# Performance work log

Hardware: AMD Instinct MI355X
Metric: run time of the kernel (lower is better)

## Reference

```python
import jax, jax.numpy as jnp
import numpy as np

DIM = 1024
DEPTH = 4
HEADS = 16
DIM_HEAD = 64
MLP = 4096
INNER = HEADS * DIM_HEAD  # == DIM, so to_out projection present
SCALE = DIM_HEAD ** -0.5
EPS = 1e-5


def layernorm(x, g, b):
    mu = jnp.mean(x, axis=-1, keepdims=True)
    var = jnp.var(x, axis=-1, keepdims=True)
    return (x - mu) * jax.lax.rsqrt(var + EPS) * g + b


def setup_inputs() -> dict:
    key = jax.random.key(0)
    ks = jax.random.split(key, 12)
    B, N = 4, 1024
    s = lambda fan: 1.0 / np.sqrt(fan)
    inp = {
        "x": jax.random.normal(ks[0], (B, N, DIM), jnp.float32),
        "Wqkv": jax.random.normal(ks[1], (DEPTH, DIM, 3 * INNER), jnp.float32) * s(DIM),
        "Wout": jax.random.normal(ks[2], (DEPTH, INNER, DIM), jnp.float32) * s(INNER),
        "bout": jnp.zeros((DEPTH, DIM), jnp.float32),
        "ln1_g": jnp.ones((DEPTH, DIM), jnp.float32),
        "ln1_b": jnp.zeros((DEPTH, DIM), jnp.float32),
        "W1": jax.random.normal(ks[3], (DEPTH, DIM, MLP), jnp.float32) * s(DIM),
        "b1": jnp.zeros((DEPTH, MLP), jnp.float32),
        "W2": jax.random.normal(ks[4], (DEPTH, MLP, DIM), jnp.float32) * s(MLP),
        "b2": jnp.zeros((DEPTH, DIM), jnp.float32),
        "ln2_g": jnp.ones((DEPTH, DIM), jnp.float32),
        "ln2_b": jnp.zeros((DEPTH, DIM), jnp.float32),
        "masks_np": jax.random.randint(ks[5], (B, N), 0, 2, jnp.int32),
        "masks_bert": jax.random.randint(ks[6], (B, N), 0, 2, jnp.int32),
    }
    return inp


def reference(x, Wqkv, Wout, bout, ln1_g, ln1_b, W1, b1, W2, b2, ln2_g, ln2_b,
              masks_np, masks_bert):
    B, N, _ = x.shape
    # pairwise mask: masks_np_[b,i,j] = masks_np[b,i] * masks_np[b,j]
    np_pair = (masks_np[:, :, None] * masks_np[:, None, :])[:, None, :, :]  # [B,1,N,N]
    bert_col = masks_bert[:, None, None, :]                                  # [B,1,1,N]
    for l in range(DEPTH):
        # --- PreNorm masked attention ---
        h = layernorm(x, ln1_g[l], ln1_b[l])
        qkv = h @ Wqkv[l]                                   # [B,N,3*INNER]
        q, k, v = jnp.split(qkv, 3, axis=-1)
        rs = lambda t: t.reshape(B, N, HEADS, DIM_HEAD).transpose(0, 2, 1, 3)
        q, k, v = rs(q), rs(k), rs(v)                       # [B,H,N,D]
        dots = jnp.einsum('bhid,bhjd->bhij', q, k) * SCALE  # [B,H,N,N]
        dots = jnp.where(np_pair == 0, -1000.0, dots)
        dots = jnp.where(bert_col == 1, -1000.0, dots)
        attn = jax.nn.softmax(dots, axis=-1)
        out = jnp.einsum('bhij,bhjd->bhid', attn, v)        # [B,H,N,D]
        out = out.transpose(0, 2, 1, 3).reshape(B, N, INNER)
        x = x + (out @ Wout[l] + bout[l])
        # --- PreNorm FFN ---
        h2 = layernorm(x, ln2_g[l], ln2_b[l])
        h2 = jax.nn.gelu(h2 @ W1[l] + b1[l], approximate=False)
        x = x + (h2 @ W2[l] + b2[l])
    return x
```

## Files before the change

### kernel.cpp

```cpp
#include <hip/hip_runtime.h>
#include <hip/hip_bf16.h>

#define DEPTH 4
#define HEADS 16
#define DIMH  64
#define DIM   1024
#define MLPD  4096
#define NTOK  1024
#define BATCH 4
#define ROWS  (BATCH*NTOK)
#define SCALE 0.125f

typedef float f32x4 __attribute__((ext_vector_type(4)));
typedef short s16x8 __attribute__((ext_vector_type(8)));

#define MFMA(a,b,c) __builtin_amdgcn_mfma_f32_16x16x32_bf16((a),(b),(c),0,0,0)

__device__ __forceinline__ unsigned short f2bf(float f){
  union{ __hip_bfloat16 h; unsigned short u; } x; x.h = __float2bfloat16(f); return x.u;
}
__device__ __forceinline__ float bf2f(unsigned short u){
  return __uint_as_float(((unsigned)u)<<16);
}

__device__ __forceinline__ void async16(const void* g, void* l){
  __builtin_amdgcn_global_load_lds(
      (const __attribute__((address_space(1))) void*)g,
      (__attribute__((address_space(3))) void*)l, 16, 0, 0);
}

__global__ __launch_bounds__(256) void wt_kernel(const float* __restrict__ src,
    unsigned short* __restrict__ dst, int K, int N)
{
  __shared__ float t[64][65];
  int n0 = blockIdx.x*64, k0 = blockIdx.y*64;
  src += (size_t)blockIdx.z*K*N;
  dst += (size_t)blockIdx.z*N*K;
  int tid = threadIdx.x;
  int r = tid>>4, c4 = (tid&15)*4;
#pragma unroll
  for (int p=0;p<4;p++){
    int row = r + p*16;
    float4 v = *(const float4*)(src + (size_t)(k0+row)*N + n0 + c4);
    t[c4+0][row]=v.x; t[c4+1][row]=v.y; t[c4+2][row]=v.z; t[c4+3][row]=v.w;
  }
  __syncthreads();
  int rn = tid>>2, ch = tid&3;
  unsigned short o[16];
#pragma unroll
  for (int i=0;i<16;i++) o[i] = f2bf(t[rn][ch*16+i]);
  uint4* d = (uint4*)(dst + (size_t)(n0+rn)*K + k0 + ch*16);
  d[0] = ((uint4*)o)[0]; d[1] = ((uint4*)o)[1];
}

__global__ __launch_bounds__(256) void ln_kernel(const float* __restrict__ x,
    const float* __restrict__ g, const float* __restrict__ b,
    unsigned short* __restrict__ h)
{
  int row  = blockIdx.x*4 + (threadIdx.x>>6);
  int lane = threadIdx.x & 63;
  const float* xr = x + (size_t)row*DIM;
  float4 v[4]; float s=0.f, ss=0.f;
#pragma unroll
  for (int c=0;c<4;c++){
    v[c] = *(const float4*)(xr + c*256 + lane*4);
    s  += v[c].x+v[c].y+v[c].z+v[c].w;
    ss += v[c].x*v[c].x+v[c].y*v[c].y+v[c].z*v[c].z+v[c].w*v[c].w;
  }
#pragma unroll
  for (int o=1;o<64;o<<=1){ s += __shfl_xor(s,o); ss += __shfl_xor(ss,o); }
  float mu  = s*(1.f/1024.f);
  float var = ss*(1.f/1024.f) - mu*mu;
  float rstd = rsqrtf(var + 1e-5f);
#pragma unroll
  for (int c=0;c<4;c++){
    float4 gg = *(const float4*)(g + c*256 + lane*4);
    float4 bb = *(const float4*)(b + c*256 + lane*4);
    ushort4 o;
    o.x = f2bf((v[c].x-mu)*rstd*gg.x + bb.x);
    o.y = f2bf((v[c].y-mu)*rstd*gg.y + bb.y);
    o.z = f2bf((v[c].z-mu)*rstd*gg.z + bb.z);
    o.w = f2bf((v[c].w-mu)*rstd*gg.w + bb.w);
    *(ushort4*)(h + (size_t)row*DIM + c*256 + lane*4) = o;
  }
}

__global__ __launch_bounds__(256) void vtrans_kernel(
    const unsigned short* __restrict__ qkv, unsigned short* __restrict__ vT)
{
  __shared__ float t[64][65];
  int n0 = blockIdx.x*64;
  int bh = blockIdx.y; int b = bh>>4, hh = bh&15;
  int tid = threadIdx.x;
  int r = tid>>4, c4 = (tid&15)*4;
#pragma unroll
  for (int p=0;p<4;p++){
    int row = r + p*16;
    ushort4 u = *(const ushort4*)(qkv + (size_t)(b*NTOK + n0 + row)*3072 + 2048 + hh*64 + c4);
    t[c4+0][row]=bf2f(u.x); t[c4+1][row]=bf2f(u.y); t[c4+2][row]=bf2f(u.z); t[c4+3][row]=bf2f(u.w);
  }
  __syncthreads();
  int rn = tid>>2, ch = tid&3;
  unsigned short o[16];
#pragma unroll
  for (int i=0;i<16;i++) o[i] = f2bf(t[rn][ch*16+i]);
  uint4* d = (uint4*)(vT + (size_t)(bh*64 + rn)*NTOK + n0 + ch*16);
  d[0] = ((uint4*)o)[0]; d[1] = ((uint4*)o)[1];
}

template<int BN, int EPI>
__global__ __launch_bounds__(256) void gemm_kernel(
    const unsigned short* __restrict__ A,
    const unsigned short* __restrict__ Bt,
    unsigned short* __restrict__ outb,
    float* __restrict__ outf,
    const float* __restrict__ res,
    const float* __restrict__ bias,
    int M, int N, int K, int ldout)
{
  constexpr int BM=128, BK=64;
  constexpr int NT = BN/32;
  __shared__ unsigned short As[BM*BK];
  __shared__ unsigned short Bs[BN*BK];
  int tid = threadIdx.x, lane = tid&63, w = tid>>6;
  int wm = w&1, wn = w>>1;

  int gn  = N/BN;
  int nwg = (M/BM)*gn;
  int bid = blockIdx.x;
  int id  = (nwg%8==0) ? ((bid&7)*(nwg>>3) + (bid>>3)) : bid;
  int m0 = (id/gn)*BM, n0 = (id%gn)*BN;

  f32x4 acc[4][NT] = {};

  for (int k0=0; k0<K; k0+=BK){
    __syncthreads();
#pragma unroll
    for (int i=0;i<4;i++){
      int off = w*4096 + i*1024 + lane*16;
      int row = off>>7, p = (off&127)>>4;
      async16(A + (size_t)(m0+row)*K + k0 + ((p^(row&7))<<3),
              (char*)As + w*4096 + i*1024);
    }
#pragma unroll
    for (int i=0;i<NT;i++){
      int off = w*(BN*32) + i*1024 + lane*16;
      int row = off>>7, p = (off&127)>>4;
      async16(Bt + (size_t)(n0+row)*K + k0 + ((p^(row&7))<<3),
              (char*)Bs + w*(BN*32) + i*1024);
    }
    __syncthreads();
#pragma unroll
    for (int ks=0;ks<2;ks++){
      s16x8 a[4], bfr[NT];
#pragma unroll
      for (int mt=0;mt<4;mt++){
        int row = wm*64 + mt*16 + (lane&15);
        int c = (ks*4 + (lane>>4)) ^ (row&7);
        a[mt] = *(const s16x8*)((const char*)As + row*128 + c*16);
      }
#pragma unroll
      for (int nt=0;nt<NT;nt++){
        int row = wn*(BN/2) + nt*16 + (lane&15);
        int c = (ks*4 + (lane>>4)) ^ (row&7);
        bfr[nt] = *(const s16x8*)((const char*)Bs + row*128 + c*16);
      }
#pragma unroll
      for (int mt=0;mt<4;mt++)
#pragma unroll
        for (int nt=0;nt<NT;nt++)
          acc[mt][nt] = MFMA(a[mt], bfr[nt], acc[mt][nt]);
    }
  }

#pragma unroll
  for (int mt=0;mt<4;mt++)
#pragma unroll
    for (int nt=0;nt<NT;nt++)
#pragma unroll
      for (int r=0;r<4;r++){
        int row = m0 + wm*64 + mt*16 + ((lane>>4)<<2) + r;
        int col = n0 + wn*(BN/2) + nt*16 + (lane&15);
        float v = acc[mt][nt][r];
        if (EPI==0){
          outb[(size_t)row*ldout + col] = f2bf(v);
        } else if (EPI==1){
          float t = v + res[(size_t)row*ldout + col] + bias[col];
          outf[(size_t)row*ldout + col] = t;
        } else {
          float t = v + bias[col];
          t = 0.5f*t*(1.f + erff(t*0.70710678118f));
          outb[(size_t)row*ldout + col] = f2bf(t);
        }
      }
}

__global__ __launch_bounds__(256) void attn_kernel(
    const unsigned short* __restrict__ qkv,
    const unsigned short* __restrict__ vT,
    const int* __restrict__ mnp, const int* __restrict__ mbert,
    unsigned short* __restrict__ outb)
{
  __shared__ unsigned short Ks[64*64];
  __shared__ unsigned short Vs[64*64];
  __shared__ unsigned short Pb[4][16*64];
  __shared__ float fm[NTOK];
  int qt = blockIdx.x, bh = blockIdx.y;
  int b = bh>>4, hh = bh&15;
  int tid = threadIdx.x, lane = tid&63, w = tid>>6;

  for (int j = tid; j < NTOK; j += 256)
    fm[j] = (mnp[b*NTOK+j]==0 || mbert[b*NTOK+j]==1) ? 1.f : 0.f;

  int iA = qt*64 + w*16 + (lane&15);
  s16x8 aq[2];
#pragma unroll
  for (int ks=0;ks<2;ks++)
    aq[ks] = *(const s16x8*)(qkv + (size_t)(b*NTOK+iA)*3072 + hh*64 + ks*32 + ((lane>>4)<<3));

  bool rowm[4]; float mreg[4], lsum[4]; f32x4 o[4];
#pragma unroll
  for (int r=0;r<4;r++){
    int i = qt*64 + w*16 + ((lane>>4)<<2) + r;
    rowm[r] = (mnp[b*NTOK+i]==0);
    mreg[r] = -1e30f; lsum[r] = 0.f;
    o[r] = f32x4{0.f,0.f,0.f,0.f};
  }

  for (int kc=0; kc<16; kc++){
    int j0 = kc*64;
    __syncthreads();
#pragma unroll
    for (int i=0;i<2;i++){
      int off = w*2048 + i*1024 + lane*16;
      int row = off>>7, p = (off&127)>>4;
      async16(qkv + (size_t)(b*NTOK + j0 + row)*3072 + 1024 + hh*64 + ((p^(row&7))<<3),
              (char*)Ks + w*2048 + i*1024);
      async16(vT + (size_t)(bh*64 + row)*NTOK + j0 + ((p^(row&7))<<3),
              (char*)Vs + w*2048 + i*1024);
    }
    __syncthreads();

    f32x4 sc[4];
#pragma unroll
    for (int jt=0;jt<4;jt++){
      sc[jt] = f32x4{0.f,0.f,0.f,0.f};
#pragma unroll
      for (int ks=0;ks<2;ks++){
        int row = jt*16 + (lane&15);
        int c = (ks*4 + (lane>>4)) ^ (row&7);
        s16x8 bk = *(const s16x8*)((const char*)Ks + row*128 + c*16);
        sc[jt] = MFMA(aq[ks], bk, sc[jt]);
      }
    }
#pragma unroll
    for (int jt=0;jt<4;jt++){
      float f = fm[j0 + jt*16 + (lane&15)];
#pragma unroll
      for (int r=0;r<4;r++){
        float s = sc[jt][r]*SCALE;
        sc[jt][r] = (f!=0.f || rowm[r]) ? -1000.f : s;
      }
    }
#pragma unroll
    for (int r=0;r<4;r++){
      float mx = fmaxf(fmaxf(sc[0][r],sc[1][r]), fmaxf(sc[2][r],sc[3][r]));
#pragma unroll
      for (int ofs=8;ofs>=1;ofs>>=1) mx = fmaxf(mx, __shfl_xor(mx, ofs));
      float mnew  = fmaxf(mreg[r], mx);
      float alpha = __expf(mreg[r]-mnew);
      mreg[r] = mnew;
      float rs = 0.f;
#pragma unroll
      for (int jt=0;jt<4;jt++){ float p = __expf(sc[jt][r]-mnew); sc[jt][r]=p; rs+=p; }
#pragma unroll
      for (int ofs=8;ofs>=1;ofs>>=1) rs += __shfl_xor(rs, ofs);
      lsum[r] = lsum[r]*alpha + rs;
#pragma unroll
      for (int nt=0;nt<4;nt++) o[nt][r] *= alpha;
    }
#pragma unroll
    for (int jt=0;jt<4;jt++)
#pragma unroll
      for (int r=0;r<4;r++){
        int ir = ((lane>>4)<<2)+r, jc = jt*16+(lane&15);
        int byteoff = ir*128 + ((((jc>>3))^(ir&7))<<4) + ((jc&7)<<1);
        *((unsigned short*)((char*)Pb[w] + byteoff)) = f2bf(sc[jt][r]);
      }
#pragma unroll
    for (int ks=0;ks<2;ks++){
      int rowp = lane&15;
      int cp = (ks*4 + (lane>>4)) ^ (rowp&7);
      s16x8 ap = *(const s16x8*)((const char*)Pb[w] + rowp*128 + cp*16);
#pragma unroll
      for (int nt=0;nt<4;nt++){
        int d = nt*16 + (lane&15);
        int c = (ks*4 + (lane>>4)) ^ (d&7);
        s16x8 bv = *(const s16x8*)((const char*)Vs + d*128 + c*16);
        o[nt] = MFMA(ap, bv, o[nt]);
      }
    }
  }

#pragma unroll
  for (int r=0;r<4;r++){
    float inv = 1.f/lsum[r];
    int i = qt*64 + w*16 + ((lane>>4)<<2) + r;
#pragma unroll
    for (int nt=0;nt<4;nt++){
      int d = nt*16 + (lane&15);
      outb[(size_t)(b*NTOK+i)*DIM + hh*64 + d] = f2bf(o[nt][r]*inv);
    }
  }
}

extern "C" void kernel_launch(void* const* d_in, const int* in_sizes, int n_in,
                              void* d_out, int out_size, void* d_ws, size_t ws_size,
                              hipStream_t stream)
{
  const float* xin0 = (const float*)d_in[0];
  const float* Wqkv = (const float*)d_in[1];
  const float* Wout = (const float*)d_in[2];
  const float* bout = (const float*)d_in[3];
  const float* ln1g = (const float*)d_in[4];
  const float* ln1b = (const float*)d_in[5];
  const float* W1   = (const float*)d_in[6];
  const float* b1   = (const float*)d_in[7];
  const float* W2   = (const float*)d_in[8];
  const float* b2   = (const float*)d_in[9];
  const float* ln2g = (const float*)d_in[10];
  const float* ln2b = (const float*)d_in[11];
  const int*   mnp  = (const int*)d_in[12];
  const int*   mbt  = (const int*)d_in[13];
  float* out = (float*)d_out;

  unsigned short* Wqkv_t = (unsigned short*)d_ws;
  unsigned short* Wout_t = Wqkv_t + (size_t)4*3072*1024;
  unsigned short* W1_t   = Wout_t + (size_t)4*1024*1024;
  unsigned short* W2_t   = W1_t   + (size_t)4*4096*1024;
  float*          x      = (float*)(W2_t + (size_t)4*1024*4096);
  unsigned short* hbuf   = (unsigned short*)(x + (size_t)ROWS*DIM);
  unsigned short* qkvb   = hbuf  + (size_t)ROWS*DIM;
  unsigned short* vTb    = qkvb  + (size_t)ROWS*3072;
  unsigned short* attnb  = vTb   + (size_t)ROWS*DIM;
  unsigned short* gbuf   = attnb + (size_t)ROWS*DIM;

  wt_kernel<<<dim3(3072/64,1024/64,4),256,0,stream>>>(Wqkv, Wqkv_t, 1024, 3072);
  wt_kernel<<<dim3(1024/64,1024/64,4),256,0,stream>>>(Wout, Wout_t, 1024, 1024);
  wt_kernel<<<dim3(4096/64,1024/64,4),256,0,stream>>>(W1,   W1_t,   1024, 4096);
  wt_kernel<<<dim3(1024/64,4096/64,4),256,0,stream>>>(W2,   W2_t,   4096, 1024);

  for (int l=0;l<4;l++){
    const float* xres = (l==0) ? xin0 : x;
    ln_kernel<<<1024,256,0,stream>>>(xres, ln1g+l*DIM, ln1b+l*DIM, hbuf);
    gemm_kernel<128,0><<<768,256,0,stream>>>(hbuf, Wqkv_t + (size_t)l*3072*1024,
        qkvb, nullptr, nullptr, nullptr, ROWS, 3072, 1024, 3072);
    vtrans_kernel<<<dim3(16,64),256,0,stream>>>(qkvb, vTb);
    attn_kernel<<<dim3(16,64),256,0,stream>>>(qkvb, vTb, mnp, mbt, attnb);
    gemm_kernel<64,1><<<512,256,0,stream>>>(attnb, Wout_t + (size_t)l*1024*1024,
        nullptr, x, xres, bout+l*DIM, ROWS, 1024, 1024, 1024);
    ln_kernel<<<1024,256,0,stream>>>(x, ln2g+l*DIM, ln2b+l*DIM, hbuf);
    gemm_kernel<128,2><<<1024,256,0,stream>>>(hbuf, W1_t + (size_t)l*4096*1024,
        gbuf, nullptr, nullptr, b1+l*MLPD, ROWS, 4096, 1024, 4096);
    float* xo = (l==3) ? out : x;
    gemm_kernel<64,1><<<512,256,0,stream>>>(gbuf, W2_t + (size_t)l*1024*4096,
        nullptr, xo, x, b2+l*DIM, ROWS, 1024, 4096, 1024);
  }
}
```

Before: 1.258 ms.

## Add 256x256 pipelined GEMM for QKV/FFN1 and double-buffer attention K/V loads

```diff
diff --git a/kernel.cpp b/kernel.cpp
--- a/kernel.cpp
+++ b/kernel.cpp
@@ -195,14 +195,149 @@
       }
 }
 
+template<int EPI>
+__global__ __launch_bounds__(512,2) void gemm256_kernel(
+    const unsigned short* __restrict__ A,
+    const unsigned short* __restrict__ Bt,
+    unsigned short* __restrict__ outb,
+    const float* __restrict__ bias,
+    int M, int N, int K, int ldout)
+{
+  __shared__ unsigned short lds[2][2][256*64];
+  const int tid = threadIdx.x, lane = tid&63, w = tid>>6;
+  const int wm = w>>2, wn = w&3;
+  const int gn = N>>8;
+  const int nwg = (M>>8)*gn;
+  const int q = nwg>>3, r = nwg&7;
+  const int xc = blockIdx.x&7, od = blockIdx.x>>3;
+  const int id = (xc<r ? xc*(q+1) : r*(q+1)+(xc-r)*q) + od;
+  const int m0 = (id/gn)<<8, n0 = (id%gn)<<8;
+  const int nkt = K>>6;
+
+  f32x4 acc[8][4] = {};
+  s16x8 af[8][2];
+  s16x8 bf[2][2];
+
+  auto stage = [&](int bsel, int half, int kt){
+    const unsigned short* src = (half<2) ? A : Bt;
+    const int base0 = (half<2) ? m0 : n0;
+    const int rbase = (half&1)<<7;
+    char* dstbase = (char*)lds[bsel][half>>1] + (rbase<<7);
+#pragma unroll
+    for (int i=0;i<2;i++){
+      int off  = ((w<<1)+i)<<10;
+      int loff = off + lane*16;
+      int row  = loff>>7, p = (loff&127)>>4;
+      async16(src + (size_t)(base0+rbase+row)*K + (kt<<6) + ((p^(row&7))<<3),
+              dstbase + off);
+    }
+  };
+
+#define LDA(mt,ks) { int rw=(wm<<7)+((mt)<<4)+(lane&15); int pc=(((ks)<<2)+(lane>>4))^(rw&7); \
+  af[mt][ks] = *(const s16x8*)((const char*)lds[cur][0] + rw*128 + (pc<<4)); }
+#define LDB(j,nt,ks) { int rw=(wn<<6)+((nt)<<4)+(lane&15); int pc=(((ks)<<2)+(lane>>4))^(rw&7); \
+  bf[j][ks] = *(const s16x8*)((const char*)lds[cur][1] + rw*128 + (pc<<4)); }
+
+  stage(0,0,0); stage(0,1,0); stage(0,2,0); stage(0,3,0);
+  stage(1,0,1); stage(1,1,1);
+  asm volatile("s_waitcnt vmcnt(4)" ::: "memory");
+  __builtin_amdgcn_s_barrier();
+
+  for (int t=0; t<nkt; ++t){
+    const int cur = t&1, nxt = cur^1;
+#pragma unroll
+    for (int mt=0;mt<4;mt++){ LDA(mt,0); LDA(mt,1); }
+#pragma unroll
+    for (int nt=0;nt<2;nt++){ LDB(nt,nt,0); LDB(nt,nt,1); }
+    if (t+1<nkt) stage(nxt,2,t+1);
+    __builtin_amdgcn_s_barrier();
+    asm volatile("s_waitcnt lgkmcnt(0)" ::: "memory");
+    __builtin_amdgcn_sched_barrier(0);
+    __builtin_amdgcn_s_setprio(1);
+#pragma unroll
+    for (int mt=0;mt<4;mt++)
+#pragma unroll
+      for (int nt=0;nt<2;nt++){
+        acc[mt][nt] = MFMA(af[mt][0], bf[nt][0], acc[mt][nt]);
+        acc[mt][nt] = MFMA(af[mt][1], bf[nt][1], acc[mt][nt]);
+      }
+    __builtin_amdgcn_s_setprio(0);
+    __builtin_amdgcn_s_barrier();
+#pragma unroll
+    for (int mt=4;mt<8;mt++){ LDA(mt,0); LDA(mt,1); }
+    if (t+1<nkt) stage(nxt,3,t+1);
+    __builtin_amdgcn_s_barrier();
+    asm volatile("s_waitcnt lgkmcnt(0)" ::: "memory");
+    __builtin_amdgcn_sched_barrier(0);
+    __builtin_amdgcn_s_setprio(1);
+#pragma unroll
+    for (int mt=4;mt<8;mt++)
+#pragma unroll
+      for (int nt=0;nt<2;nt++){
+        acc[mt][nt] = MFMA(af[mt][0], bf[nt][0], acc[mt][nt]);
+        acc[mt][nt] = MFMA(af[mt][1], bf[nt][1], acc[mt][nt]);
+      }
+    __builtin_amdgcn_s_setprio(0);
+    __builtin_amdgcn_s_barrier();
+#pragma unroll
+    for (int nt=0;nt<2;nt++){ LDB(nt,nt+2,0); LDB(nt,nt+2,1); }
+    if (t+2<nkt) stage(cur,0,t+2);
+    __builtin_amdgcn_s_barrier();
+    asm volatile("s_waitcnt lgkmcnt(0)" ::: "memory");
+    __builtin_amdgcn_sched_barrier(0);
+    __builtin_amdgcn_s_setprio(1);
+#pragma unroll
+    for (int mt=0;mt<4;mt++)
+#pragma unroll
+      for (int nt=0;nt<2;nt++){
+        acc[mt][nt+2] = MFMA(af[mt][0], bf[nt][0], acc[mt][nt+2]);
+        acc[mt][nt+2] = MFMA(af[mt][1], bf[nt][1], acc[mt][nt+2]);
+      }
+    __builtin_amdgcn_s_setprio(0);
+    __builtin_amdgcn_s_barrier();
+    if (t+2<nkt) stage(cur,1,t+2);
+    __builtin_amdgcn_s_barrier();
+    __builtin_amdgcn_s_setprio(1);
+#pragma unroll
+    for (int mt=4;mt<8;mt++)
+#pragma unroll
+      for (int nt=0;nt<2;nt++){
+        acc[mt][nt+2] = MFMA(af[mt][0], bf[nt][0], acc[mt][nt+2]);
+        acc[mt][nt+2] = MFMA(af[mt][1], bf[nt][1], acc[mt][nt+2]);
+      }
+    __builtin_amdgcn_s_setprio(0);
+    if (t+2<nkt) asm volatile("s_waitcnt vmcnt(4)" ::: "memory");
+    else         asm volatile("s_waitcnt vmcnt(0)" ::: "memory");
+    __builtin_amdgcn_s_barrier();
+  }
+#undef LDA
+#undef LDB
+
+#pragma unroll
+  for (int mt=0;mt<8;mt++)
+#pragma unroll
+    for (int nt=0;nt<4;nt++)
+#pragma unroll
+      for (int rr=0;rr<4;rr++){
+        int row = m0 + (wm<<7) + (mt<<4) + ((lane>>4)<<2) + rr;
+        int col = n0 + (wn<<6) + (nt<<4) + (lane&15);
+        float v = acc[mt][nt][rr];
+        if (EPI==2){
+          v += bias[col];
+          v = 0.5f*v*(1.f + erff(v*0.70710678118f));
+        }
+        outb[(size_t)row*ldout + col] = f2bf(v);
+      }
+}
+
 __global__ __launch_bounds__(256) void attn_kernel(
     const unsigned short* __restrict__ qkv,
     const unsigned short* __restrict__ vT,
     const int* __restrict__ mnp, const int* __restrict__ mbert,
     unsigned short* __restrict__ outb)
 {
-  __shared__ unsigned short Ks[64*64];
-  __shared__ unsigned short Vs[64*64];
+  __shared__ unsigned short Ks[2][64*64];
+  __shared__ unsigned short Vs[2][64*64];
   __shared__ unsigned short Pb[4][16*64];
   __shared__ float fm[NTOK];
   int qt = blockIdx.x, bh = blockIdx.y;
@@ -226,22 +361,34 @@
     mreg[r] = -1e30f; lsum[r] = 0.f;
     o[r] = f32x4{0.f,0.f,0.f,0.f};
   }
+  __syncthreads();
+
+  auto stageKV = [&](int bufi, int kc){
+    int j0 = kc<<6;
+#pragma unroll
+    for (int i=0;i<2;i++){
+      int off  = w*2048 + i*1024;
+      int loff = off + lane*16;
+      int row  = loff>>7, p = (loff&127)>>4;
+      async16(qkv + (size_t)(b*NTOK + j0 + row)*3072 + 1024 + hh*64 + ((p^(row&7))<<3),
+              (char*)Ks[bufi] + off);
+      async16(vT + (size_t)(bh*64 + row)*NTOK + j0 + ((p^(row&7))<<3),
+              (char*)Vs[bufi] + off);
+    }
+  };
+
+  stageKV(0,0);
 
   for (int kc=0; kc<16; kc++){
+    int cur = kc&1;
     int j0 = kc*64;
-    __syncthreads();
-#pragma unroll
-    for (int i=0;i<2;i++){
-      int off = w*2048 + i*1024 + lane*16;
-      int row = off>>7, p = (off&127)>>4;
-      async16(qkv + (size_t)(b*NTOK + j0 + row)*3072 + 1024 + hh*64 + ((p^(row&7))<<3),
-              (char*)Ks + w*2048 + i*1024);
-      async16(vT + (size_t)(bh*64 + row)*NTOK + j0 + ((p^(row&7))<<3),
-              (char*)Vs + w*2048 + i*1024);
-    }
-    __syncthreads();
+    if (kc<15) stageKV(cur^1, kc+1);
+    if (kc<15) asm volatile("s_waitcnt vmcnt(4)" ::: "memory");
+    else       asm volatile("s_waitcnt vmcnt(0)" ::: "memory");
+    __builtin_amdgcn_s_barrier();
 
     f32x4 sc[4];
+    __builtin_amdgcn_s_setprio(1);
 #pragma unroll
     for (int jt=0;jt<4;jt++){
       sc[jt] = f32x4{0.f,0.f,0.f,0.f};
@@ -249,10 +396,11 @@
       for (int ks=0;ks<2;ks++){
         int row = jt*16 + (lane&15);
         int c = (ks*4 + (lane>>4)) ^ (row&7);
-        s16x8 bk = *(const s16x8*)((const char*)Ks + row*128 + c*16);
+        s16x8 bk = *(const s16x8*)((const char*)Ks[cur] + row*128 + c*16);
         sc[jt] = MFMA(aq[ks], bk, sc[jt]);
       }
     }
+    __builtin_amdgcn_s_setprio(0);
 #pragma unroll
     for (int jt=0;jt<4;jt++){
       float f = fm[j0 + jt*16 + (lane&15)];
@@ -273,8 +421,6 @@
       float rs = 0.f;
 #pragma unroll
       for (int jt=0;jt<4;jt++){ float p = __expf(sc[jt][r]-mnew); sc[jt][r]=p; rs+=p; }
-#pragma unroll
-      for (int ofs=8;ofs>=1;ofs>>=1) rs += __shfl_xor(rs, ofs);
       lsum[r] = lsum[r]*alpha + rs;
 #pragma unroll
       for (int nt=0;nt<4;nt++) o[nt][r] *= alpha;
@@ -287,6 +433,7 @@
         int byteoff = ir*128 + ((((jc>>3))^(ir&7))<<4) + ((jc&7)<<1);
         *((unsigned short*)((char*)Pb[w] + byteoff)) = f2bf(sc[jt][r]);
       }
+    __builtin_amdgcn_s_setprio(1);
 #pragma unroll
     for (int ks=0;ks<2;ks++){
       int rowp = lane&15;
@@ -296,14 +443,18 @@
       for (int nt=0;nt<4;nt++){
         int d = nt*16 + (lane&15);
         int c = (ks*4 + (lane>>4)) ^ (d&7);
-        s16x8 bv = *(const s16x8*)((const char*)Vs + d*128 + c*16);
+        s16x8 bv = *(const s16x8*)((const char*)Vs[cur] + d*128 + c*16);
         o[nt] = MFMA(ap, bv, o[nt]);
       }
     }
+    __builtin_amdgcn_s_setprio(0);
+    __builtin_amdgcn_s_barrier();
   }
 
 #pragma unroll
   for (int r=0;r<4;r++){
+#pragma unroll
+    for (int ofs=8;ofs>=1;ofs>>=1) lsum[r] += __shfl_xor(lsum[r], ofs);
     float inv = 1.f/lsum[r];
     int i = qt*64 + w*16 + ((lane>>4)<<2) + r;
 #pragma unroll
@@ -353,15 +504,15 @@
   for (int l=0;l<4;l++){
     const float* xres = (l==0) ? xin0 : x;
     ln_kernel<<<1024,256,0,stream>>>(xres, ln1g+l*DIM, ln1b+l*DIM, hbuf);
-    gemm_kernel<128,0><<<768,256,0,stream>>>(hbuf, Wqkv_t + (size_t)l*3072*1024,
-        qkvb, nullptr, nullptr, nullptr, ROWS, 3072, 1024, 3072);
+    gemm256_kernel<0><<<192,512,0,stream>>>(hbuf, Wqkv_t + (size_t)l*3072*1024,
+        qkvb, nullptr, ROWS, 3072, 1024, 3072);
     vtrans_kernel<<<dim3(16,64),256,0,stream>>>(qkvb, vTb);
     attn_kernel<<<dim3(16,64),256,0,stream>>>(qkvb, vTb, mnp, mbt, attnb);
     gemm_kernel<64,1><<<512,256,0,stream>>>(attnb, Wout_t + (size_t)l*1024*1024,
         nullptr, x, xres, bout+l*DIM, ROWS, 1024, 1024, 1024);
     ln_kernel<<<1024,256,0,stream>>>(x, ln2g+l*DIM, ln2b+l*DIM, hbuf);
-    gemm_kernel<128,2><<<1024,256,0,stream>>>(hbuf, W1_t + (size_t)l*4096*1024,
-        gbuf, nullptr, nullptr, b1+l*MLPD, ROWS, 4096, 1024, 4096);
+    gemm256_kernel<2><<<256,512,0,stream>>>(hbuf, W1_t + (size_t)l*4096*1024,
+        gbuf, b1+l*MLPD, ROWS, 4096, 1024, 4096);
     float* xo = (l==3) ? out : x;
     gemm_kernel<64,1><<<512,256,0,stream>>>(gbuf, W2_t + (size_t)l*1024*4096,
         nullptr, xo, x, b2+l*DIM, ROWS, 1024, 4096, 1024);
```

Result: faster. 1.217 ms (-3.3%).
